# Kernel tuning notes

Hardware: AMD Instinct MI355X
Metric: run time of the kernel (lower is better)

The kernel has to match this reference:

```python
import jax, jax.numpy as jnp
import numpy as np

B, U1, U2 = 4, 2048, 2048
C = 256      # in_feat_dim
F = 256      # feat_dim
M = 4        # num_modes
D = C // M   # attention_mode_dim = 64
ATTN_CLIP = 500.0
LN_EPS = 1e-12


def setup_inputs() -> dict:
    key = jax.random.key(0)
    ks = jax.random.split(key, 8)
    s = 0.02  # base_initializer_range
    inp = {
        "query_feat": jax.random.normal(ks[0], (B, U1, C), jnp.float32),
        "key_feat": jax.random.normal(ks[1], (B, U2, C), jnp.float32),
        "Wq": jax.random.normal(ks[2], (M * D, C), jnp.float32) * s,
        "bq": jnp.zeros((M * D,), jnp.float32),
    }
    # tie_qk_scheme='shared': key linear shares query weights
    inp["Wk"] = inp["Wq"]
    inp["bk"] = inp["bq"]
    inp["Wv"] = jax.random.normal(ks[3], (M * F, C), jnp.float32) * s  # first_linear, v_has_bias=False
    inp["W_mid"] = jax.random.normal(ks[4], (F, F), jnp.float32) * s   # MMSharedMid shared_linear
    inp["b_mid"] = jnp.zeros((F,), jnp.float32)
    inp["W_out"] = jax.random.normal(ks[5], (M, F, F), jnp.float32) * s  # grouped 1x1 conv, per mode
    inp["b_out"] = jnp.zeros((M, F), jnp.float32)
    inp["ln_g"] = jnp.ones((F,), jnp.float32)   # resout LayerNorm
    inp["ln_b"] = jnp.zeros((F,), jnp.float32)
    inp["W_score"] = jax.random.normal(ks[6], (1, F), jnp.float32) * s  # LearnedSoftAggregate
    inp["b_score"] = jnp.zeros((1,), jnp.float32)
    return inp


def _layer_norm(x, g, b):
    mu = jnp.mean(x, axis=-1, keepdims=True)
    var = jnp.var(x, axis=-1, keepdims=True)
    return (x - mu) * jax.lax.rsqrt(var + LN_EPS) * g + b


def reference(query_feat, key_feat, Wq, bq, Wk, bk, Wv, W_mid, b_mid,
              W_out, b_out, ln_g, ln_b, W_score, b_score):
    # --- tied-QK multi-mode attention ---
    q = (query_feat @ Wq.T + bq).reshape(B, U1, M, D)
    k = (key_feat @ Wk.T + bk).reshape(B, U2, M, D)
    scores = jnp.einsum('bimd,bjmd->bmij', q, k) / jnp.sqrt(jnp.float32(D))
    scores = jnp.clip(scores, -ATTN_CLIP, ATTN_CLIP)  # attn_clip
    probs = jax.nn.softmax(scores, axis=-1)           # [B, M, U1, U2]

    # --- ExpandedFeatTrans: value projection + fusion ---
    v = (key_feat @ Wv.T).reshape(B, U2, M, F)        # first_linear (no bias)
    fused = jnp.einsum('bmij,bjmf->bmif', probs, v)   # [B, M, U1, F]

    # MMSharedMid: shared linear over F + gelu (dropout = identity in eval)
    mid = jax.nn.gelu(fused @ W_mid.T + b_mid, approximate=False)

    # MMPrivateOutput: per-mode grouped 1x1 conv; NOTE the original code computes
    # x_comb = x + shortcut but then layer-norms x (shortcut dropped) - kept faithful.
    out = jnp.einsum('bmif,mgf->bmig', mid, W_out) + b_out[None, :, None, :]
    out = _layer_norm(out, ln_g, ln_b)                # [B, M, U1, F]

    # LearnedSoftAggregate over modes (group_dim=1, keepdim=False)
    mode_scores = out @ W_score.T + b_score           # [B, M, U1, 1]
    mode_probs = jax.nn.softmax(mode_scores, axis=1)
    return jnp.sum(out * mode_probs, axis=1)          # [B, U1, F]
```

## Files before the change

### kernel.cpp

```cpp
#include <hip/hip_runtime.h>

typedef __attribute__((ext_vector_type(8))) short short8;
typedef __attribute__((ext_vector_type(4))) float f32x4;
typedef __attribute__((ext_vector_type(16))) float f32x16;
typedef unsigned short u16t;
typedef unsigned int u32t;

#define MFMA16(a, b, c) __builtin_amdgcn_mfma_f32_16x16x32_bf16((a), (b), (c), 0, 0, 0)
#define MFMA32(a, b, c) __builtin_amdgcn_mfma_f32_32x32x16_bf16((a), (b), (c), 0, 0, 0)

__device__ __forceinline__ u16t f2bf(float f) {
  u32t u = __float_as_uint(f);
  u32t r = u + 0x7fffu + ((u >> 16) & 1u);
  return (u16t)(r >> 16);
}
__device__ __forceinline__ float bf2f(u16t b) {
  return __uint_as_float(((u32t)b) << 16);
}
__device__ __forceinline__ short8 pack8(float4 a0, float4 a1) {
  short8 r;
  r[0] = (short)f2bf(a0.x); r[1] = (short)f2bf(a0.y);
  r[2] = (short)f2bf(a0.z); r[3] = (short)f2bf(a0.w);
  r[4] = (short)f2bf(a1.x); r[5] = (short)f2bf(a1.y);
  r[6] = (short)f2bf(a1.z); r[7] = (short)f2bf(a1.w);
  return r;
}
__device__ __forceinline__ u32t packrhu(float a, float b) {
  u32t ua = __float_as_uint(a) + 0x8000u;
  u32t ub = __float_as_uint(b) + 0x8000u;
  return (ua >> 16) | (ub & 0xffff0000u);
}

__global__ void cvt_kernel(const float* __restrict__ src, u16t* __restrict__ dst, int n) {
  int i = blockIdx.x * 256 + threadIdx.x;
  if (i < n) dst[i] = f2bf(src[i]);
}

__global__ __launch_bounds__(256) void proj_gemm(
    const float* __restrict__ A, const float* __restrict__ W,
    const float* __restrict__ bias, float scale,
    u16t* __restrict__ out, int mode) {
  __shared__ __align__(16) u16t As[64 * 72];
  __shared__ __align__(16) u16t Ws[64 * 72];
  const int tid = threadIdx.x;
  const int w = tid >> 6, lane = tid & 63, quad = lane >> 4, l15 = lane & 15;
  const int l31 = lane & 31, h8 = (lane >> 5) * 8;
  const int rt = blockIdx.x * 64;
  const int ct = blockIdx.y * 64;
  const int wrow = (w >> 1) * 32, wcol = (w & 1) * 32;
  const int r2 = tid >> 3, c8 = tid & 7;

  const f32x4 fzero = {0.f, 0.f, 0.f, 0.f};
  f32x4 acc[2][2];
#pragma unroll
  for (int i = 0; i < 2; i++)
#pragma unroll
    for (int j = 0; j < 2; j++) acc[i][j] = fzero;

  for (int kt = 0; kt < 4; ++kt) {
    __syncthreads();
#pragma unroll
    for (int hh = 0; hh < 2; ++hh) {
      int rr = r2 + hh * 32;
      const float4* pa = (const float4*)(A + (size_t)(rt + rr) * 256 + kt * 64 + c8 * 8);
      const float4* pw = (const float4*)(W + (size_t)(ct + rr) * 256 + kt * 64 + c8 * 8);
      float4 w0 = pw[0], w1 = pw[1];
      w0.x *= scale; w0.y *= scale; w0.z *= scale; w0.w *= scale;
      w1.x *= scale; w1.y *= scale; w1.z *= scale; w1.w *= scale;
      *(short8*)&As[rr * 72 + c8 * 8] = pack8(pa[0], pa[1]);
      *(short8*)&Ws[rr * 72 + c8 * 8] = pack8(w0, w1);
    }
    __syncthreads();
#pragma unroll
    for (int ks = 0; ks < 2; ++ks) {
      short8 af0 = *(const short8*)&As[(wrow + l15) * 72 + ks * 32 + quad * 8];
      short8 af1 = *(const short8*)&As[(wrow + 16 + l15) * 72 + ks * 32 + quad * 8];
      short8 bw0 = *(const short8*)&Ws[(wcol + l15) * 72 + ks * 32 + quad * 8];
      short8 bw1 = *(const short8*)&Ws[(wcol + 16 + l15) * 72 + ks * 32 + quad * 8];
      acc[0][0] = MFMA16(af0, bw0, acc[0][0]);
      acc[0][1] = MFMA16(af0, bw1, acc[0][1]);
      acc[1][0] = MFMA16(af1, bw0, acc[1][0]);
      acc[1][1] = MFMA16(af1, bw1, acc[1][1]);
    }
  }

  __syncthreads();
  u16t* Cs = As;
  if (mode == 0) {
#pragma unroll
    for (int i = 0; i < 2; i++) {
      int rl = wrow + i * 16 + quad * 4;
#pragma unroll
      for (int j = 0; j < 2; j++) {
        int cl = wcol + j * 16 + l15;
        float bv = bias ? bias[ct + cl] * scale : 0.f;
#pragma unroll
        for (int rg = 0; rg < 4; ++rg)
          Cs[(rl + rg) * 72 + cl] = f2bf(acc[i][j][rg] + bv);
      }
    }
  } else {
#pragma unroll
    for (int i = 0; i < 2; i++) {
      int rl = wrow + i * 16 + quad * 4;
#pragma unroll
      for (int j = 0; j < 2; j++) {
        int cl = wcol + j * 16 + l15;
        ushort4 pk;
        pk.x = f2bf(acc[i][j][0]);
        pk.y = f2bf(acc[i][j][1]);
        pk.z = f2bf(acc[i][j][2]);
        pk.w = f2bf(acc[i][j][3]);
        *(ushort4*)&Cs[cl * 72 + rl] = pk;
      }
    }
  }
  __syncthreads();

#pragma unroll
  for (int t2 = 0; t2 < 2; ++t2) {
    short8 frag = *(const short8*)&Cs[(t2 * 32 + l31) * 72 + w * 16 + h8];
    size_t base;
    if (mode == 0) {
      int b = rt >> 11, m = blockIdx.y;
      int it32 = ((rt & 2047) >> 5) + t2;
      base = (((size_t)(b * 4 + m) * 64 + it32) * 4 + w) * 512;
    } else {
      int b = rt >> 11, m = blockIdx.y >> 2;
      int fb = ((blockIdx.y & 3) << 1) + t2;
      int jt16 = ((rt & 2047) >> 4) + w;
      base = (((size_t)(b * 4 + m) * 8 + fb) * 128 + jt16) * 512;
    }
    *(short8*)(out + base + lane * 8) = frag;
  }
}

__global__ __launch_bounds__(256, 3) void attn_kernel(
    const u16t* __restrict__ Qf, const u16t* __restrict__ Kf,
    const u16t* __restrict__ Vf,
    const u16t* __restrict__ Wmid, const u16t* __restrict__ Wout,
    const float* __restrict__ b_mid, const float* __restrict__ b_out,
    const float* __restrict__ ln_g, const float* __restrict__ ln_b,
    const float* __restrict__ Wsc, const float* __restrict__ b_sc,
    u16t* __restrict__ out_ln, float* __restrict__ scoresWS) {
  __shared__ __align__(16) u16t smF[32 * 264];
  __shared__ __align__(16) u16t smP[2][32 * 132];
  __shared__ float smL[128];
  __shared__ float smR[128];
  __shared__ float smS[64];
  const int tid = threadIdx.x;
  const int w = tid >> 6, lane = tid & 63, quad = lane >> 4, l15 = lane & 15;
  const int l31 = lane & 31, h = lane >> 5;
  const int L = blockIdx.y * 64 + blockIdx.x;
  const int xcd = L & 7, slot = L >> 3;
  const int bm = xcd * 2 + (slot >> 6);
  const int it32 = slot & 63;
  const int m = bm & 3;
  const int q0 = it32 * 32;

  const size_t lane8 = (size_t)lane * 8;

  const u16t* qbase = Qf + ((size_t)(bm * 64 + it32) * 4) * 512 + lane8;
  short8 qf4[4];
#pragma unroll
  for (int ksd = 0; ksd < 4; ++ksd)
    qf4[ksd] = *(const short8*)(qbase + ksd * 512);

  const u16t* kbase = Kf + ((size_t)bm * 256) * 512 + lane8;
  const u16t* vbase = Vf + ((size_t)(bm * 8 + 2 * w) * 128) * 512 + lane8;

  f32x16 facc[2];
#pragma unroll
  for (int j = 0; j < 2; j++)
#pragma unroll
    for (int r = 0; r < 16; r++) facc[j][r] = 0.f;
  float lsum = 0.f;

  short8 kf4[4];
#pragma unroll
  for (int ksd = 0; ksd < 4; ++ksd)
    kf4[ksd] = *(const short8*)(kbase + (size_t)w * 2048 + ksd * 512);

#pragma unroll 1
  for (int t = 0; t < 16; ++t) {
    u16t* Pb = &smP[t & 1][0];
    f32x16 sacc;
#pragma unroll
    for (int r = 0; r < 16; r++) sacc[r] = 0.f;
#pragma unroll
    for (int ksd = 0; ksd < 4; ++ksd)
      sacc = MFMA32(kf4[ksd], qf4[ksd], sacc);

    float ls = 0.f;
#pragma unroll
    for (int tt = 0; tt < 8; ++tt) {
      float p0 = __expf(sacc[2 * tt]);
      float p1 = __expf(sacc[2 * tt + 1]);
      ls += p0 + p1;
      const int jl = ((2 * tt) & 3) + 8 * ((2 * tt) >> 2) + 4 * h;
      *(u32t*)&Pb[l31 * 132 + w * 32 + jl] = packrhu(p0, p1);
    }
    lsum += ls;

    __syncthreads();

    if (t < 15) {
      const int jt32n = (t + 1) * 4 + w;
#pragma unroll
      for (int ksd = 0; ksd < 4; ++ksd)
        kf4[ksd] = *(const short8*)(kbase + (size_t)jt32n * 2048 + ksd * 512);
    }
#pragma unroll
    for (int jj = 0; jj < 4; ++jj) {
      short8 vf[2][2];
#pragma unroll
      for (int fb = 0; fb < 2; ++fb)
#pragma unroll
        for (int ks2 = 0; ks2 < 2; ++ks2)
          vf[fb][ks2] = *(const short8*)(vbase + ((size_t)fb * 128 + (t * 8 + jj * 2 + ks2)) * 512);
      short8 bbL[2];
#pragma unroll
      for (int ks2 = 0; ks2 < 2; ++ks2)
        bbL[ks2] = *(const short8*)&Pb[l31 * 132 + jj * 32 + ks2 * 16 + h * 8];
      facc[0] = MFMA32(vf[0][0], bbL[0], facc[0]);
      facc[0] = MFMA32(vf[0][1], bbL[1], facc[0]);
      facc[1] = MFMA32(vf[1][0], bbL[0], facc[1]);
      facc[1] = MFMA32(vf[1][1], bbL[1], facc[1]);
    }
  }

  lsum += __shfl_xor(lsum, 32);
  if (h == 0) smL[w * 32 + l31] = lsum;
  __syncthreads();
  float inv = 1.f / (smL[l31] + smL[32 + l31] + smL[64 + l31] + smL[96 + l31]);

#pragma unroll
  for (int fb = 0; fb < 2; ++fb) {
#pragma unroll
    for (int g = 0; g < 4; ++g) {
      int fbase = w * 64 + fb * 32 + 8 * g + 4 * h;
      ushort4 pk4;
      pk4.x = f2bf(facc[fb][4 * g + 0] * inv);
      pk4.y = f2bf(facc[fb][4 * g + 1] * inv);
      pk4.z = f2bf(facc[fb][4 * g + 2] * inv);
      pk4.w = f2bf(facc[fb][4 * g + 3] * inv);
      *(ushort4*)&smF[l31 * 264 + fbase] = pk4;
    }
  }
  __syncthreads();

  const int rgrp = w >> 1, ch = w & 1;
  const int rowq = rgrp * 16 + quad * 4;
  const f32x4 fz4 = {0.f, 0.f, 0.f, 0.f};

  f32x4 macc[8];
#pragma unroll
  for (int i = 0; i < 8; i++) macc[i] = fz4;
  for (int kc = 0; kc < 8; ++kc) {
    short8 af = *(const short8*)&smF[(rgrp * 16 + l15) * 264 + kc * 32 + quad * 8];
#pragma unroll
    for (int nb = 0; nb < 8; ++nb) {
      short8 bw = *(const short8*)(Wmid + (size_t)(ch * 128 + nb * 16 + l15) * 256 + kc * 32 + quad * 8);
      macc[nb] = MFMA16(af, bw, macc[nb]);
    }
  }
#pragma unroll
  for (int nb = 0; nb < 8; ++nb) {
    int c = ch * 128 + nb * 16 + l15;
    float bmv = b_mid[c];
#pragma unroll
    for (int rg = 0; rg < 4; ++rg) {
      float x = macc[nb][rg] + bmv;
      macc[nb][rg] = 0.5f * x * (1.f + erff(x * 0.70710678118654752f));
    }
  }
  __syncthreads();
#pragma unroll
  for (int nb = 0; nb < 8; ++nb)
#pragma unroll
    for (int rg = 0; rg < 4; ++rg)
      smF[(rowq + rg) * 264 + ch * 128 + nb * 16 + l15] = f2bf(macc[nb][rg]);
  __syncthreads();

  const u16t* Wo = Wout + (size_t)m * 65536;
  f32x4 oacc[8];
#pragma unroll
  for (int i = 0; i < 8; i++) oacc[i] = fz4;
  for (int kc = 0; kc < 8; ++kc) {
    short8 af = *(const short8*)&smF[(rgrp * 16 + l15) * 264 + kc * 32 + quad * 8];
#pragma unroll
    for (int nb = 0; nb < 8; ++nb) {
      short8 bw = *(const short8*)(Wo + (size_t)(ch * 128 + nb * 16 + l15) * 256 + kc * 32 + quad * 8);
      oacc[nb] = MFMA16(af, bw, oacc[nb]);
    }
  }

  float sum[4] = {0, 0, 0, 0}, sq[4] = {0, 0, 0, 0};
#pragma unroll
  for (int nb = 0; nb < 8; ++nb) {
    int c = ch * 128 + nb * 16 + l15;
    float bo = b_out[m * 256 + c];
#pragma unroll
    for (int rg = 0; rg < 4; ++rg) {
      float x = oacc[nb][rg] + bo;
      oacc[nb][rg] = x;
      sum[rg] += x;
      sq[rg] += x * x;
    }
  }
#pragma unroll
  for (int rg = 0; rg < 4; ++rg) {
    float s = sum[rg], s2 = sq[rg];
    s += __shfl_xor(s, 1); s += __shfl_xor(s, 2); s += __shfl_xor(s, 4); s += __shfl_xor(s, 8);
    s2 += __shfl_xor(s2, 1); s2 += __shfl_xor(s2, 2); s2 += __shfl_xor(s2, 4); s2 += __shfl_xor(s2, 8);
    if (l15 == 0) {
      smR[(rowq + rg) + 32 * ch] = s;
      smR[64 + (rowq + rg) + 32 * ch] = s2;
    }
  }
  __syncthreads();
  float mu[4], rstd[4];
#pragma unroll
  for (int rg = 0; rg < 4; ++rg) {
    int r = rowq + rg;
    float s = smR[r] + smR[r + 32];
    float s2 = smR[64 + r] + smR[64 + r + 32];
    float mean = s * (1.f / 256.f);
    float var = s2 * (1.f / 256.f) - mean * mean;
    mu[rg] = mean;
    rstd[rg] = rsqrtf(var + 1e-12f);
  }

  float scp[4] = {0, 0, 0, 0};
#pragma unroll
  for (int nb = 0; nb < 8; ++nb) {
    int c = ch * 128 + nb * 16 + l15;
    float g = ln_g[c], bb2 = ln_b[c], wsv = Wsc[c];
#pragma unroll
    for (int rg = 0; rg < 4; ++rg) {
      float xn = (oacc[nb][rg] - mu[rg]) * rstd[rg] * g + bb2;
      out_ln[((size_t)bm * 2048 + (q0 + rowq + rg)) * 256 + c] = f2bf(xn);
      scp[rg] += xn * wsv;
    }
  }
#pragma unroll
  for (int rg = 0; rg < 4; ++rg) {
    float s = scp[rg];
    s += __shfl_xor(s, 1); s += __shfl_xor(s, 2); s += __shfl_xor(s, 4); s += __shfl_xor(s, 8);
    if (l15 == 0) smS[(rowq + rg) + 32 * ch] = s;
  }
  __syncthreads();
  if (ch == 0 && l15 == 0) {
#pragma unroll
    for (int rg = 0; rg < 4; ++rg) {
      int r = rowq + rg;
      scoresWS[bm * 2048 + q0 + r] = smS[r] + smS[r + 32] + b_sc[0];
    }
  }
}

__global__ __launch_bounds__(256) void agg_kernel(
    const u16t* __restrict__ out_ln, const float* __restrict__ scoresWS,
    float* __restrict__ out) {
  const int row = blockIdx.x;
  const int c = threadIdx.x;
  const int b = row >> 11, i = row & 2047;
  float s0 = scoresWS[(b * 4 + 0) * 2048 + i];
  float s1 = scoresWS[(b * 4 + 1) * 2048 + i];
  float s2 = scoresWS[(b * 4 + 2) * 2048 + i];
  float s3 = scoresWS[(b * 4 + 3) * 2048 + i];
  float mx = fmaxf(fmaxf(s0, s1), fmaxf(s2, s3));
  float e0 = __expf(s0 - mx), e1 = __expf(s1 - mx), e2 = __expf(s2 - mx), e3 = __expf(s3 - mx);
  float inv = 1.f / (e0 + e1 + e2 + e3);
  float acc = e0 * inv * bf2f(out_ln[((size_t)(b * 4 + 0) * 2048 + i) * 256 + c]) +
              e1 * inv * bf2f(out_ln[((size_t)(b * 4 + 1) * 2048 + i) * 256 + c]) +
              e2 * inv * bf2f(out_ln[((size_t)(b * 4 + 2) * 2048 + i) * 256 + c]) +
              e3 * inv * bf2f(out_ln[((size_t)(b * 4 + 3) * 2048 + i) * 256 + c]);
  out[(size_t)row * 256 + c] = acc;
}

extern "C" void kernel_launch(void* const* d_in, const int* in_sizes, int n_in,
                              void* d_out, int out_size, void* d_ws, size_t ws_size,
                              hipStream_t stream) {
  (void)in_sizes; (void)n_in; (void)out_size; (void)ws_size;
  const float* query = (const float*)d_in[0];
  const float* key   = (const float*)d_in[1];
  const float* Wq    = (const float*)d_in[2];
  const float* bq    = (const float*)d_in[3];
  const float* Wv    = (const float*)d_in[6];
  const float* Wm    = (const float*)d_in[7];
  const float* bmid  = (const float*)d_in[8];
  const float* Wo    = (const float*)d_in[9];
  const float* bo    = (const float*)d_in[10];
  const float* lng   = (const float*)d_in[11];
  const float* lnb   = (const float*)d_in[12];
  const float* Wsc   = (const float*)d_in[13];
  const float* bsc   = (const float*)d_in[14];

  char* p = (char*)d_ws;
  u16t* QfB = (u16t*)p; p += (size_t)2097152 * 2;
  u16t* KfB = (u16t*)p; p += (size_t)2097152 * 2;
  u16t* VfB = (u16t*)p; p += (size_t)8388608 * 2;
  u16t* WmB = (u16t*)p; p += (size_t)65536 * 2;
  u16t* WoB = (u16t*)p; p += (size_t)262144 * 2;
  u16t* outLn = (u16t*)p; p += (size_t)8388608 * 2;
  float* scWS = (float*)p; p += (size_t)32768 * 4;

  cvt_kernel<<<256, 256, 0, stream>>>(Wm, WmB, 65536);
  cvt_kernel<<<1024, 256, 0, stream>>>(Wo, WoB, 262144);

  proj_gemm<<<dim3(128, 4), 256, 0, stream>>>(query, Wq, bq, 0.125f, QfB, 0);
  proj_gemm<<<dim3(128, 4), 256, 0, stream>>>(key, Wq, bq, 1.0f, KfB, 0);
  proj_gemm<<<dim3(128, 16), 256, 0, stream>>>(key, Wv, nullptr, 1.0f, VfB, 1);

  attn_kernel<<<dim3(64, 16), 256, 0, stream>>>(QfB, KfB, VfB, WmB, WoB,
                                                bmid, bo, lng, lnb, Wsc, bsc,
                                                outLn, scWS);

  agg_kernel<<<8192, 256, 0, stream>>>(outLn, scWS, (float*)d_out);
}
```

Measured before the change: 255.2 us.

## Merge prep kernels into one launch and widen attention key tile to 256

Folds the two weight-conversion kernels and the three projection GEMMs into a single prep kernel that dispatches by block index, cutting four launches and their tail gaps. The attention loop now handles 256 keys per iteration (two 32-wide score tiles per wave) instead of 128, halving the number of block-wide barriers and doubling independent score MFMAs per step. The P buffer grows and is aliased with the fused-feature buffer in shared memory, which raises register and LDS pressure and may lower occupancy.

```diff
diff --git a/kernel.cpp b/kernel.cpp
--- a/kernel.cpp
+++ b/kernel.cpp
@@ -31,22 +31,16 @@
   return (ua >> 16) | (ub & 0xffff0000u);
 }
 
-__global__ void cvt_kernel(const float* __restrict__ src, u16t* __restrict__ dst, int n) {
-  int i = blockIdx.x * 256 + threadIdx.x;
-  if (i < n) dst[i] = f2bf(src[i]);
-}
-
-__global__ __launch_bounds__(256) void proj_gemm(
+__device__ __forceinline__ void proj_dev(
     const float* __restrict__ A, const float* __restrict__ W,
     const float* __restrict__ bias, float scale,
-    u16t* __restrict__ out, int mode) {
-  __shared__ __align__(16) u16t As[64 * 72];
-  __shared__ __align__(16) u16t Ws[64 * 72];
+    u16t* __restrict__ out, int mode, int bx, int by,
+    u16t* As, u16t* Ws) {
   const int tid = threadIdx.x;
   const int w = tid >> 6, lane = tid & 63, quad = lane >> 4, l15 = lane & 15;
   const int l31 = lane & 31, h8 = (lane >> 5) * 8;
-  const int rt = blockIdx.x * 64;
-  const int ct = blockIdx.y * 64;
+  const int rt = bx * 64;
+  const int ct = by * 64;
   const int wrow = (w >> 1) * 32, wcol = (w & 1) * 32;
   const int r2 = tid >> 3, c8 = tid & 7;
 
@@ -122,17 +116,52 @@
     short8 frag = *(const short8*)&Cs[(t2 * 32 + l31) * 72 + w * 16 + h8];
     size_t base;
     if (mode == 0) {
-      int b = rt >> 11, m = blockIdx.y;
+      int b = rt >> 11, m = by;
       int it32 = ((rt & 2047) >> 5) + t2;
       base = (((size_t)(b * 4 + m) * 64 + it32) * 4 + w) * 512;
     } else {
-      int b = rt >> 11, m = blockIdx.y >> 2;
-      int fb = ((blockIdx.y & 3) << 1) + t2;
+      int b = rt >> 11, m = by >> 2;
+      int fb = ((by & 3) << 1) + t2;
       int jt16 = ((rt & 2047) >> 4) + w;
       base = (((size_t)(b * 4 + m) * 8 + fb) * 128 + jt16) * 512;
     }
     *(short8*)(out + base + lane * 8) = frag;
   }
+}
+
+__global__ __launch_bounds__(256) void prep_kernel(
+    const float* __restrict__ query, const float* __restrict__ key,
+    const float* __restrict__ Wq, const float* __restrict__ bq,
+    const float* __restrict__ Wv, const float* __restrict__ Wm,
+    const float* __restrict__ Wo,
+    u16t* __restrict__ WmB, u16t* __restrict__ WoB,
+    u16t* __restrict__ QfB, u16t* __restrict__ KfB, u16t* __restrict__ VfB) {
+  __shared__ __align__(16) u16t As[64 * 72];
+  __shared__ __align__(16) u16t Ws[64 * 72];
+  const int blk = blockIdx.x;
+  const int tid = threadIdx.x;
+  if (blk < 256) {
+    int i = blk * 256 + tid;
+    WmB[i] = f2bf(Wm[i]);
+    return;
+  }
+  if (blk < 1280) {
+    int i = (blk - 256) * 256 + tid;
+    WoB[i] = f2bf(Wo[i]);
+    return;
+  }
+  const float *A, *W, *bias;
+  float scale;
+  u16t* out;
+  int mode, local;
+  if (blk < 1792) {
+    local = blk - 1280; A = query; W = Wq; bias = bq; scale = 0.125f; out = QfB; mode = 0;
+  } else if (blk < 2304) {
+    local = blk - 1792; A = key; W = Wq; bias = bq; scale = 1.0f; out = KfB; mode = 0;
+  } else {
+    local = blk - 2304; A = key; W = Wv; bias = nullptr; scale = 1.0f; out = VfB; mode = 1;
+  }
+  proj_dev(A, W, bias, scale, out, mode, local & 127, local >> 7, As, Ws);
 }
 
 __global__ __launch_bounds__(256, 3) void attn_kernel(
@@ -143,15 +172,14 @@
     const float* __restrict__ ln_g, const float* __restrict__ ln_b,
     const float* __restrict__ Wsc, const float* __restrict__ b_sc,
     u16t* __restrict__ out_ln, float* __restrict__ scoresWS) {
-  __shared__ __align__(16) u16t smF[32 * 264];
-  __shared__ __align__(16) u16t smP[2][32 * 132];
+  __shared__ __align__(16) u16t smBig[16640];
   __shared__ float smL[128];
   __shared__ float smR[128];
   __shared__ float smS[64];
   const int tid = threadIdx.x;
   const int w = tid >> 6, lane = tid & 63, quad = lane >> 4, l15 = lane & 15;
   const int l31 = lane & 31, h = lane >> 5;
-  const int L = blockIdx.y * 64 + blockIdx.x;
+  const int L = blockIdx.x;
   const int xcd = L & 7, slot = L >> 3;
   const int bm = xcd * 2 + (slot >> 6);
   const int it32 = slot & 63;
@@ -176,52 +204,61 @@
     for (int r = 0; r < 16; r++) facc[j][r] = 0.f;
   float lsum = 0.f;
 
-  short8 kf4[4];
-#pragma unroll
-  for (int ksd = 0; ksd < 4; ++ksd)
-    kf4[ksd] = *(const short8*)(kbase + (size_t)w * 2048 + ksd * 512);
+  short8 kfA[4], kfB[4];
+#pragma unroll
+  for (int ksd = 0; ksd < 4; ++ksd) {
+    kfA[ksd] = *(const short8*)(kbase + (size_t)w * 2048 + ksd * 512);
+    kfB[ksd] = *(const short8*)(kbase + (size_t)(w + 4) * 2048 + ksd * 512);
+  }
 
 #pragma unroll 1
-  for (int t = 0; t < 16; ++t) {
-    u16t* Pb = &smP[t & 1][0];
-    f32x16 sacc;
-#pragma unroll
-    for (int r = 0; r < 16; r++) sacc[r] = 0.f;
-#pragma unroll
-    for (int ksd = 0; ksd < 4; ++ksd)
-      sacc = MFMA32(kf4[ksd], qf4[ksd], sacc);
+  for (int t = 0; t < 8; ++t) {
+    u16t* Pb = &smBig[(t & 1) * 8320];
+    f32x16 saccA, saccB;
+#pragma unroll
+    for (int r = 0; r < 16; r++) { saccA[r] = 0.f; saccB[r] = 0.f; }
+#pragma unroll
+    for (int ksd = 0; ksd < 4; ++ksd) {
+      saccA = MFMA32(kfA[ksd], qf4[ksd], saccA);
+      saccB = MFMA32(kfB[ksd], qf4[ksd], saccB);
+    }
 
     float ls = 0.f;
 #pragma unroll
     for (int tt = 0; tt < 8; ++tt) {
-      float p0 = __expf(sacc[2 * tt]);
-      float p1 = __expf(sacc[2 * tt + 1]);
-      ls += p0 + p1;
       const int jl = ((2 * tt) & 3) + 8 * ((2 * tt) >> 2) + 4 * h;
-      *(u32t*)&Pb[l31 * 132 + w * 32 + jl] = packrhu(p0, p1);
+      float a0 = __expf(saccA[2 * tt]);
+      float a1 = __expf(saccA[2 * tt + 1]);
+      float b0 = __expf(saccB[2 * tt]);
+      float b1 = __expf(saccB[2 * tt + 1]);
+      ls += a0 + a1 + b0 + b1;
+      *(u32t*)&Pb[l31 * 260 + w * 32 + jl] = packrhu(a0, a1);
+      *(u32t*)&Pb[l31 * 260 + (w + 4) * 32 + jl] = packrhu(b0, b1);
     }
     lsum += ls;
 
     __syncthreads();
 
-    if (t < 15) {
-      const int jt32n = (t + 1) * 4 + w;
-#pragma unroll
-      for (int ksd = 0; ksd < 4; ++ksd)
-        kf4[ksd] = *(const short8*)(kbase + (size_t)jt32n * 2048 + ksd * 512);
-    }
-#pragma unroll
-    for (int jj = 0; jj < 4; ++jj) {
+    if (t < 7) {
+      const int jA = (t + 1) * 8 + w, jB = jA + 4;
+#pragma unroll
+      for (int ksd = 0; ksd < 4; ++ksd) {
+        kfA[ksd] = *(const short8*)(kbase + (size_t)jA * 2048 + ksd * 512);
+        kfB[ksd] = *(const short8*)(kbase + (size_t)jB * 2048 + ksd * 512);
+      }
+    }
+#pragma unroll
+    for (int jj = 0; jj < 8; ++jj) {
       short8 vf[2][2];
 #pragma unroll
       for (int fb = 0; fb < 2; ++fb)
 #pragma unroll
         for (int ks2 = 0; ks2 < 2; ++ks2)
-          vf[fb][ks2] = *(const short8*)(vbase + ((size_t)fb * 128 + (t * 8 + jj * 2 + ks2)) * 512);
+          vf[fb][ks2] = *(const short8*)(vbase + ((size_t)fb * 128 + (t * 16 + jj * 2 + ks2)) * 512);
       short8 bbL[2];
 #pragma unroll
       for (int ks2 = 0; ks2 < 2; ++ks2)
-        bbL[ks2] = *(const short8*)&Pb[l31 * 132 + jj * 32 + ks2 * 16 + h * 8];
+        bbL[ks2] = *(const short8*)&Pb[l31 * 260 + jj * 32 + ks2 * 16 + h * 8];
       facc[0] = MFMA32(vf[0][0], bbL[0], facc[0]);
       facc[0] = MFMA32(vf[0][1], bbL[1], facc[0]);
       facc[1] = MFMA32(vf[1][0], bbL[0], facc[1]);
@@ -234,6 +271,7 @@
   __syncthreads();
   float inv = 1.f / (smL[l31] + smL[32 + l31] + smL[64 + l31] + smL[96 + l31]);
 
+  u16t* smF = smBig;
 #pragma unroll
   for (int fb = 0; fb < 2; ++fb) {
 #pragma unroll
@@ -406,16 +444,12 @@
   u16t* outLn = (u16t*)p; p += (size_t)8388608 * 2;
   float* scWS = (float*)p; p += (size_t)32768 * 4;
 
-  cvt_kernel<<<256, 256, 0, stream>>>(Wm, WmB, 65536);
-  cvt_kernel<<<1024, 256, 0, stream>>>(Wo, WoB, 262144);
-
-  proj_gemm<<<dim3(128, 4), 256, 0, stream>>>(query, Wq, bq, 0.125f, QfB, 0);
-  proj_gemm<<<dim3(128, 4), 256, 0, stream>>>(key, Wq, bq, 1.0f, KfB, 0);
-  proj_gemm<<<dim3(128, 16), 256, 0, stream>>>(key, Wv, nullptr, 1.0f, VfB, 1);
-
-  attn_kernel<<<dim3(64, 16), 256, 0, stream>>>(QfB, KfB, VfB, WmB, WoB,
-                                                bmid, bo, lng, lnb, Wsc, bsc,
-                                                outLn, scWS);
+  prep_kernel<<<4352, 256, 0, stream>>>(query, key, Wq, bq, Wv, Wm, Wo,
+                                        WmB, WoB, QfB, KfB, VfB);
+
+  attn_kernel<<<1024, 256, 0, stream>>>(QfB, KfB, VfB, WmB, WoB,
+                                        bmid, bo, lng, lnb, Wsc, bsc,
+                                        outLn, scWS);
 
   agg_kernel<<<8192, 256, 0, stream>>>(outLn, scWS, (float*)d_out);
 }
```

After: 247.1 us. 3.2% less time.
